# Kernel tuning notes

Measured on AMD Instinct MI355X. Metric: run time of the kernel, lower is better.

Reference implementation:

```python
import jax, jax.numpy as jnp
import numpy as np

B, T, D, HS = 8, 2048, 1024, 64


def setup_inputs() -> dict:
    key = jax.random.key(0)
    ks = jax.random.split(key, 7)
    return {
        "x": jax.random.normal(ks[0], (B, T, D), dtype=jnp.float32),
        "Wq": jax.random.normal(ks[1], (D, HS), dtype=jnp.float32) / np.sqrt(D),
        "bq": jax.random.normal(ks[2], (HS,), dtype=jnp.float32) * 0.01,
        "Wk": jax.random.normal(ks[3], (D, HS), dtype=jnp.float32) / np.sqrt(D),
        "bk": jax.random.normal(ks[4], (HS,), dtype=jnp.float32) * 0.01,
        "Wv": jax.random.normal(ks[5], (D, HS), dtype=jnp.float32) / np.sqrt(D),
        "bv": jax.random.normal(ks[6], (HS,), dtype=jnp.float32) * 0.01,
    }


def reference(x, Wq, bq, Wk, bk, Wv, bv):
    # Q,K,V projections: [B,T,D] @ [D,HS] -> [B,T,HS]
    Q = x @ Wq + bq
    K = x @ Wk + bk
    V = x @ Wv + bv
    # raw scores [B,T,T]
    scores = jnp.einsum("bqh,bkh->bqk", Q, K)
    # causal mask applied BEFORE scaling (as in the original; -inf is scale-invariant)
    causal = jnp.tril(jnp.ones((T, T), dtype=bool))
    scores = jnp.where(causal[None, :, :], scores, -jnp.inf)
    scores = scores / jnp.sqrt(jnp.asarray(HS, dtype=scores.dtype))
    attn = jax.nn.softmax(scores, axis=-1)
    # dropout is identity in eval mode (deterministic reference)
    return jnp.einsum("bqk,bkh->bqh", attn, V)
```

## Files before the change

kernel.cpp:

```cpp
#include <hip/hip_runtime.h>
#include <hip/hip_bf16.h>

typedef __bf16 bf16x8 __attribute__((ext_vector_type(8)));
typedef __bf16 bf16x4 __attribute__((ext_vector_type(4)));
typedef float  f32x4  __attribute__((ext_vector_type(4)));

#define B_  8
#define T_  2048
#define D_  1024
#define HS_ 64


__global__ __launch_bounds__(256) void pack_w(
    const float* __restrict__ Wq, const float* __restrict__ Wk,
    const float* __restrict__ Wv, __bf16* __restrict__ Wp)
{
    const int t    = blockIdx.x * 256 + threadIdx.x;
    const int lane = t & 63;
    const int pg   = t >> 6;
    const int s    = pg & 3;
    const int c    = (pg >> 2) & 31;
    const int p    = pg >> 7;
    const int m16  = lane & 15;
    const int quad = lane >> 4;

    const float* W = (p == 0) ? Wq : (p == 1) ? Wk : Wv;
    const float* src = W + (size_t)(c * 32 + quad * 8) * 64 + s * 16 + m16;
    bf16x8 frag;
    #pragma unroll
    for (int j = 0; j < 8; ++j) frag[j] = (__bf16)src[(size_t)j * 64];
    *(bf16x8*)(Wp + (size_t)pg * 512 + lane * 8) = frag;
}

__global__ __launch_bounds__(256) void qkv_fused(
    const float* __restrict__ x,
    const __bf16* __restrict__ Wp,
    const float* __restrict__ bq, const float* __restrict__ bk,
    const float* __restrict__ bv,
    __bf16* __restrict__ Q, __bf16* __restrict__ K, __bf16* __restrict__ Vt)
{
    __shared__ alignas(16) unsigned char Smem[36864];

    const int rt   = blockIdx.x;
    const int wave = threadIdx.x >> 6;
    const int lane = threadIdx.x & 63;
    const int m16  = lane & 15;
    const int quad = lane >> 4;
    const int row0 = rt * 16;

    __bf16* Xs = (__bf16*)(Smem + wave * 8448);

    {
        const float* xsrc = x + (size_t)row0 * 1024 + wave * 256;
        const int sr = lane >> 5;
        const int sc = (lane & 31) * 8;
        #pragma unroll
        for (int i = 0; i < 8; ++i) {
            const int r = i * 2 + sr;
            f32x4 v0 = *(const f32x4*)(xsrc + (size_t)r * 1024 + sc);
            f32x4 v1 = *(const f32x4*)(xsrc + (size_t)r * 1024 + sc + 4);
            bf16x8 w;
            #pragma unroll
            for (int e = 0; e < 4; ++e) { w[e] = (__bf16)v0[e]; w[4 + e] = (__bf16)v1[e]; }
            *(bf16x8*)&Xs[r * 264 + sc] = w;
        }
    }
    __builtin_amdgcn_wave_barrier();

    f32x4 acc[3][4];
    #pragma unroll
    for (int p = 0; p < 3; ++p)
        #pragma unroll
        for (int s = 0; s < 4; ++s) acc[p][s] = {0.f, 0.f, 0.f, 0.f};

    for (int k0 = 0; k0 < 256; k0 += 32) {
        bf16x8 a = *(const bf16x8*)&Xs[m16 * 264 + k0 + quad * 8];
        const int cbase = wave * 8 + (k0 >> 5);

        bf16x8 bf[12];
        #pragma unroll
        for (int ps = 0; ps < 12; ++ps) {
            const int p = ps >> 2, s = ps & 3;
            bf[ps] = *(const bf16x8*)(Wp +
                ((size_t)((p * 32 + cbase) * 4 + s) << 9) + lane * 8);
        }
        __builtin_amdgcn_sched_barrier(0);

        #pragma unroll
        for (int ps = 0; ps < 12; ++ps)
            acc[ps >> 2][ps & 3] =
                __builtin_amdgcn_mfma_f32_16x16x32_bf16(a, bf[ps], acc[ps >> 2][ps & 3], 0, 0, 0);
    }

    f32x4* Red = (f32x4*)Smem;
    __syncthreads();
    if (wave != 0) {
        #pragma unroll
        for (int p = 0; p < 3; ++p)
            #pragma unroll
            for (int s = 0; s < 4; ++s)
                Red[((wave - 1) * 12 + p * 4 + s) * 64 + lane] = acc[p][s];
    }
    __syncthreads();
    if (wave != 0) return;

    #pragma unroll
    for (int p = 0; p < 3; ++p)
        #pragma unroll
        for (int s = 0; s < 4; ++s) {
            f32x4 sum = acc[p][s];
            #pragma unroll
            for (int w = 0; w < 3; ++w) {
                f32x4 v = Red[(w * 12 + p * 4 + s) * 64 + lane];
                #pragma unroll
                for (int e = 0; e < 4; ++e) sum[e] += v[e];
            }
            acc[p][s] = sum;
        }

    #pragma unroll
    for (int s = 0; s < 4; ++s) {
        const int h = s * 16 + m16;
        const float bia = bq[h];
        #pragma unroll
        for (int r = 0; r < 4; ++r)
            Q[(size_t)(row0 + quad * 4 + r) * 64 + h] = (__bf16)(acc[0][s][r] + bia);
    }
    #pragma unroll
    for (int s = 0; s < 4; ++s) {
        const int h = s * 16 + m16;
        const float bia = bk[h];
        #pragma unroll
        for (int r = 0; r < 4; ++r)
            K[(size_t)(row0 + quad * 4 + r) * 64 + h] = (__bf16)(acc[1][s][r] + bia);
    }
    {
        const int bidx = row0 >> 11;
        const int t0   = (row0 & 2047) + quad * 4;
        #pragma unroll
        for (int s = 0; s < 4; ++s) {
            const int h = s * 16 + m16;
            const float bia = bv[h];
            bf16x4 pack;
            #pragma unroll
            for (int r = 0; r < 4; ++r) pack[r] = (__bf16)(acc[2][s][r] + bia);
            *(bf16x4*)(Vt + (size_t)bidx * (HS_ * T_) + (size_t)h * T_ + t0) = pack;
        }
    }
}

__global__ __launch_bounds__(256) void attn_fused(
    const __bf16* __restrict__ Q,
    const __bf16* __restrict__ K,
    const __bf16* __restrict__ Vt,
    float* __restrict__ O)
{
    __shared__ alignas(16) __bf16 Klds[8 * 512];
    __shared__ alignas(16) __bf16 Vlds[8 * 512];

    const int qt = blockIdx.x;
    const int b  = blockIdx.y;

    const int tid  = threadIdx.x;
    const int wave = tid >> 6;
    const int lane = tid & 63;
    const int m16  = lane & 15;
    const int quad = lane >> 4;

    const __bf16* Qb = Q  + (size_t)b * T_ * HS_;
    const __bf16* Kb = K  + (size_t)b * T_ * HS_;
    const __bf16* Vb = Vt + (size_t)b * HS_ * T_;

    const int q0   = qt * 64 + wave * 16;
    const int qrow = q0 + m16;

    bf16x8 qb0 = *(const bf16x8*)(Qb + (size_t)qrow * 64 + quad * 8);
    bf16x8 qb1 = *(const bf16x8*)(Qb + (size_t)qrow * 64 + 32 + quad * 8);

    int koffL[2], voffL[2];
    const __bf16* kgb[2];
    const __bf16* vgb[2];
    #pragma unroll
    for (int i = 0; i < 2; ++i) {
        const int p    = i * 256 + tid;
        const int trow = p >> 3;
        const int tcol = p & 7;
        const int snb  = ((trow >> 5) << 1) | ((trow >> 2) & 1);
        const int mk   = (((trow >> 3) & 3) << 2) | (trow & 3);
        koffL[i] = ((((snb << 1) | (tcol >> 2)) << 6) + (tcol & 3) * 16 + mk) * 8;
        voffL[i] = (((((trow >> 4) << 1) | (tcol >> 2)) << 6) + (tcol & 3) * 16 + (trow & 15)) * 8;
        kgb[i] = Kb + (size_t)trow * 64 + tcol * 8;
        vgb[i] = Vb + (size_t)trow * T_ + tcol * 8;
    }

    f32x4 o[4];
    #pragma unroll
    for (int hs = 0; hs < 4; ++hs) o[hs] = {0.f, 0.f, 0.f, 0.f};
    float m_run = -1e30f, l_run = 0.f;

    bf16x8 kr0 = *(const bf16x8*)(kgb[0]);
    bf16x8 kr1 = *(const bf16x8*)(kgb[1]);
    bf16x8 vr0 = *(const bf16x8*)(vgb[0]);
    bf16x8 vr1 = *(const bf16x8*)(vgb[1]);

    for (int jt = 0; jt <= qt; ++jt) {
        const int j0 = jt * 64;

        __syncthreads();
        *(bf16x8*)&Klds[koffL[0]] = kr0;
        *(bf16x8*)&Klds[koffL[1]] = kr1;
        *(bf16x8*)&Vlds[voffL[0]] = vr0;
        *(bf16x8*)&Vlds[voffL[1]] = vr1;
        __syncthreads();

        if (jt < qt) {
            const size_t nk = (size_t)(j0 + 64) * 64;
            kr0 = *(const bf16x8*)(kgb[0] + nk);
            kr1 = *(const bf16x8*)(kgb[1] + nk);
            vr0 = *(const bf16x8*)(vgb[0] + j0 + 64);
            vr1 = *(const bf16x8*)(vgb[1] + j0 + 64);
        }
        __builtin_amdgcn_sched_barrier(0);

        f32x4 s[4];
        #pragma unroll
        for (int snb = 0; snb < 4; ++snb) s[snb] = {0.f, 0.f, 0.f, 0.f};
        #pragma unroll
        for (int snb = 0; snb < 4; ++snb) {
            bf16x8 ka0 = *(const bf16x8*)&Klds[((snb * 2 + 0) * 64 + lane) * 8];
            bf16x8 ka1 = *(const bf16x8*)&Klds[((snb * 2 + 1) * 64 + lane) * 8];
            s[snb] = __builtin_amdgcn_mfma_f32_16x16x32_bf16(ka0, qb0, s[snb], 0, 0, 0);
            s[snb] = __builtin_amdgcn_mfma_f32_16x16x32_bf16(ka1, qb1, s[snb], 0, 0, 0);
        }

        float mx = -1e30f;
        #pragma unroll
        for (int snb = 0; snb < 4; ++snb) {
            const int kbase = j0 + ((snb >> 1) << 5) + (quad << 3) + ((snb & 1) << 2);
            #pragma unroll
            for (int r = 0; r < 4; ++r) {
                float v = s[snb][r] * 0.125f;
                v = (kbase + r <= qrow) ? v : -1e30f;
                s[snb][r] = v;
                mx = fmaxf(mx, v);
            }
        }
        mx = fmaxf(mx, __shfl_xor(mx, 16));
        mx = fmaxf(mx, __shfl_xor(mx, 32));

        const float newm  = fmaxf(m_run, mx);
        const float alpha = __expf(m_run - newm);
        m_run = newm;

        float rs = 0.f;
        #pragma unroll
        for (int snb = 0; snb < 4; ++snb)
            #pragma unroll
            for (int r = 0; r < 4; ++r) {
                float pv = __expf(s[snb][r] - newm);
                s[snb][r] = pv;
                rs += pv;
            }
        rs += __shfl_xor(rs, 16);
        rs += __shfl_xor(rs, 32);
        l_run = l_run * alpha + rs;

        #pragma unroll
        for (int hs = 0; hs < 4; ++hs)
            #pragma unroll
            for (int r = 0; r < 4; ++r) o[hs][r] *= alpha;

        bf16x8 pb0, pb1;
        #pragma unroll
        for (int r = 0; r < 4; ++r) {
            pb0[r]     = (__bf16)s[0][r];
            pb0[4 + r] = (__bf16)s[1][r];
            pb1[r]     = (__bf16)s[2][r];
            pb1[4 + r] = (__bf16)s[3][r];
        }

        #pragma unroll
        for (int hs = 0; hs < 4; ++hs) {
            bf16x8 va0 = *(const bf16x8*)&Vlds[((hs * 2 + 0) * 64 + lane) * 8];
            bf16x8 va1 = *(const bf16x8*)&Vlds[((hs * 2 + 1) * 64 + lane) * 8];
            o[hs] = __builtin_amdgcn_mfma_f32_16x16x32_bf16(va0, pb0, o[hs], 0, 0, 0);
            o[hs] = __builtin_amdgcn_mfma_f32_16x16x32_bf16(va1, pb1, o[hs], 0, 0, 0);
        }
    }

    const float inv = 1.f / l_run;
    float* Ob = O + ((size_t)b * T_ + (size_t)(qt * 64 + wave * 16 + m16)) * 64;
    #pragma unroll
    for (int hs = 0; hs < 4; ++hs) {
        f32x4 v;
        #pragma unroll
        for (int r = 0; r < 4; ++r) v[r] = o[hs][r] * inv;
        *(f32x4*)(Ob + hs * 16 + quad * 4) = v;
    }
}

extern "C" void kernel_launch(void* const* d_in, const int* in_sizes, int n_in,
                              void* d_out, int out_size, void* d_ws, size_t ws_size,
                              hipStream_t stream)
{
    const float* x  = (const float*)d_in[0];
    const float* Wq = (const float*)d_in[1];
    const float* bq = (const float*)d_in[2];
    const float* Wk = (const float*)d_in[3];
    const float* bk = (const float*)d_in[4];
    const float* Wv = (const float*)d_in[5];
    const float* bv = (const float*)d_in[6];
    float* out = (float*)d_out;

    __bf16* Wp = (__bf16*)d_ws;
    __bf16* Q  = Wp + 384 * 512;
    __bf16* K  = Q  + (size_t)B_ * T_ * HS_;
    __bf16* Vt = K  + (size_t)B_ * T_ * HS_;

    pack_w<<<96, 256, 0, stream>>>(Wq, Wk, Wv, Wp);
    qkv_fused<<<1024, 256, 0, stream>>>(x, Wp, bq, bk, bv, Q, K, Vt);
    attn_fused<<<dim3(32, 8), 256, 0, stream>>>(Q, K, Vt, out);
}
```

Baseline: 158.2 us.

## Balance causal attention work by pairing short and long query tiles per block

The attention kernel now uses 128-thread blocks that each handle 32 query rows. Each block processes two 32-row tiles in sequence, one early and one late (2*s and 126-2*s), so every block does about the same causal work instead of the last blocks doing far more. The LDS layout for K and V gains an XOR swizzle to cut bank conflicts on the MFMA operand reads. K/V tiles are shared by only 2 waves now, so reuse per load drops, and the grid still has only 256 blocks.

```diff
diff --git a/kernel.cpp b/kernel.cpp
--- a/kernel.cpp
+++ b/kernel.cpp
@@ -149,16 +149,16 @@
     }
 }
 
-__global__ __launch_bounds__(256) void attn_fused(
+__global__ __launch_bounds__(128) void attn_fused(
     const __bf16* __restrict__ Q,
     const __bf16* __restrict__ K,
     const __bf16* __restrict__ Vt,
     float* __restrict__ O)
 {
-    __shared__ alignas(16) __bf16 Klds[8 * 512];
-    __shared__ alignas(16) __bf16 Vlds[8 * 512];
-
-    const int qt = blockIdx.x;
+    __shared__ alignas(16) __bf16 Klds[4096];
+    __shared__ alignas(16) __bf16 Vlds[4096];
+
+    const int s  = blockIdx.x;
     const int b  = blockIdx.y;
 
     const int tid  = threadIdx.x;
@@ -170,133 +170,155 @@
     const __bf16* Qb = Q  + (size_t)b * T_ * HS_;
     const __bf16* Kb = K  + (size_t)b * T_ * HS_;
     const __bf16* Vb = Vt + (size_t)b * HS_ * T_;
-
-    const int q0   = qt * 64 + wave * 16;
-    const int qrow = q0 + m16;
-
-    bf16x8 qb0 = *(const bf16x8*)(Qb + (size_t)qrow * 64 + quad * 8);
-    bf16x8 qb1 = *(const bf16x8*)(Qb + (size_t)qrow * 64 + 32 + quad * 8);
-
-    int koffL[2], voffL[2];
-    const __bf16* kgb[2];
-    const __bf16* vgb[2];
-    #pragma unroll
-    for (int i = 0; i < 2; ++i) {
-        const int p    = i * 256 + tid;
-        const int trow = p >> 3;
-        const int tcol = p & 7;
+    float* Obase     = O  + (size_t)b * T_ * HS_;
+
+    const int tr0  = tid >> 3;
+    const int tcol = tid & 7;
+    const int c    = tcol & 3;
+    const int gco  = tcol >> 2;
+
+    int kOff[4], vOff[4];
+    #pragma unroll
+    for (int i = 0; i < 4; ++i) {
+        const int trow = tr0 + 16 * i;
         const int snb  = ((trow >> 5) << 1) | ((trow >> 2) & 1);
         const int mk   = (((trow >> 3) & 3) << 2) | (trow & 3);
-        koffL[i] = ((((snb << 1) | (tcol >> 2)) << 6) + (tcol & 3) * 16 + mk) * 8;
-        voffL[i] = (((((trow >> 4) << 1) | (tcol >> 2)) << 6) + (tcol & 3) * 16 + (trow & 15)) * 8;
+        const int ek   = (((snb << 1) | gco) << 9) + c * 128 + mk * 8;
+        kOff[i] = ek ^ (((ek >> 7) & 7) << 3);
+        const int ev   = ((((trow >> 4) << 1) | gco) << 9) + c * 128 + (trow & 15) * 8;
+        vOff[i] = ev ^ (((ev >> 7) & 7) << 3);
+    }
+    const __bf16* kgb[4];
+    const __bf16* vgb[4];
+    #pragma unroll
+    for (int i = 0; i < 4; ++i) {
+        const int trow = tr0 + 16 * i;
         kgb[i] = Kb + (size_t)trow * 64 + tcol * 8;
         vgb[i] = Vb + (size_t)trow * T_ + tcol * 8;
     }
 
-    f32x4 o[4];
-    #pragma unroll
-    for (int hs = 0; hs < 4; ++hs) o[hs] = {0.f, 0.f, 0.f, 0.f};
-    float m_run = -1e30f, l_run = 0.f;
-
-    bf16x8 kr0 = *(const bf16x8*)(kgb[0]);
-    bf16x8 kr1 = *(const bf16x8*)(kgb[1]);
-    bf16x8 vr0 = *(const bf16x8*)(vgb[0]);
-    bf16x8 vr1 = *(const bf16x8*)(vgb[1]);
-
-    for (int jt = 0; jt <= qt; ++jt) {
-        const int j0 = jt * 64;
-
-        __syncthreads();
-        *(bf16x8*)&Klds[koffL[0]] = kr0;
-        *(bf16x8*)&Klds[koffL[1]] = kr1;
-        *(bf16x8*)&Vlds[voffL[0]] = vr0;
-        *(bf16x8*)&Vlds[voffL[1]] = vr1;
-        __syncthreads();
-
-        if (jt < qt) {
-            const size_t nk = (size_t)(j0 + 64) * 64;
-            kr0 = *(const bf16x8*)(kgb[0] + nk);
-            kr1 = *(const bf16x8*)(kgb[1] + nk);
-            vr0 = *(const bf16x8*)(vgb[0] + j0 + 64);
-            vr1 = *(const bf16x8*)(vgb[1] + j0 + 64);
-        }
-        __builtin_amdgcn_sched_barrier(0);
-
-        f32x4 s[4];
-        #pragma unroll
-        for (int snb = 0; snb < 4; ++snb) s[snb] = {0.f, 0.f, 0.f, 0.f};
-        #pragma unroll
-        for (int snb = 0; snb < 4; ++snb) {
-            bf16x8 ka0 = *(const bf16x8*)&Klds[((snb * 2 + 0) * 64 + lane) * 8];
-            bf16x8 ka1 = *(const bf16x8*)&Klds[((snb * 2 + 1) * 64 + lane) * 8];
-            s[snb] = __builtin_amdgcn_mfma_f32_16x16x32_bf16(ka0, qb0, s[snb], 0, 0, 0);
-            s[snb] = __builtin_amdgcn_mfma_f32_16x16x32_bf16(ka1, qb1, s[snb], 0, 0, 0);
-        }
-
-        float mx = -1e30f;
-        #pragma unroll
-        for (int snb = 0; snb < 4; ++snb) {
-            const int kbase = j0 + ((snb >> 1) << 5) + (quad << 3) + ((snb & 1) << 2);
+    const int rsw0 = (lane * 8) ^ (quad << 3);
+    const int rsw1 = (lane * 8) ^ ((quad | 4) << 3);
+
+    auto phase = [&](const int h0) {
+        const int qrow  = (h0 + wave) * 16 + m16;
+        const int jtmax = h0 >> 2;
+
+        bf16x8 qb0 = *(const bf16x8*)(Qb + (size_t)qrow * 64 + quad * 8);
+        bf16x8 qb1 = *(const bf16x8*)(Qb + (size_t)qrow * 64 + 32 + quad * 8);
+
+        f32x4 o[4];
+        #pragma unroll
+        for (int hs = 0; hs < 4; ++hs) o[hs] = {0.f, 0.f, 0.f, 0.f};
+        float m_run = -1e30f, l_run = 0.f;
+
+        bf16x8 kr[4], vr[4];
+        #pragma unroll
+        for (int i = 0; i < 4; ++i) {
+            kr[i] = *(const bf16x8*)(kgb[i]);
+            vr[i] = *(const bf16x8*)(vgb[i]);
+        }
+
+        for (int jt = 0; jt <= jtmax; ++jt) {
+            const int j0 = jt * 64;
+
+            __syncthreads();
+            #pragma unroll
+            for (int i = 0; i < 4; ++i) {
+                *(bf16x8*)&Klds[kOff[i]] = kr[i];
+                *(bf16x8*)&Vlds[vOff[i]] = vr[i];
+            }
+            __syncthreads();
+
+            if (jt < jtmax) {
+                const size_t kadd = (size_t)(j0 + 64) * 64;
+                #pragma unroll
+                for (int i = 0; i < 4; ++i) {
+                    kr[i] = *(const bf16x8*)(kgb[i] + kadd);
+                    vr[i] = *(const bf16x8*)(vgb[i] + j0 + 64);
+                }
+            }
+            __builtin_amdgcn_sched_barrier(0);
+
+            f32x4 sv[4];
+            #pragma unroll
+            for (int snb = 0; snb < 4; ++snb) sv[snb] = {0.f, 0.f, 0.f, 0.f};
+            #pragma unroll
+            for (int snb = 0; snb < 4; ++snb) {
+                bf16x8 ka0 = *(const bf16x8*)&Klds[snb * 1024 + rsw0];
+                bf16x8 ka1 = *(const bf16x8*)&Klds[snb * 1024 + 512 + rsw1];
+                sv[snb] = __builtin_amdgcn_mfma_f32_16x16x32_bf16(ka0, qb0, sv[snb], 0, 0, 0);
+                sv[snb] = __builtin_amdgcn_mfma_f32_16x16x32_bf16(ka1, qb1, sv[snb], 0, 0, 0);
+            }
+
+            float mx = -1e30f;
+            #pragma unroll
+            for (int snb = 0; snb < 4; ++snb) {
+                const int kbase = j0 + ((snb >> 1) << 5) + (quad << 3) + ((snb & 1) << 2);
+                #pragma unroll
+                for (int r = 0; r < 4; ++r) {
+                    float v = sv[snb][r] * 0.125f;
+                    v = (kbase + r <= qrow) ? v : -1e30f;
+                    sv[snb][r] = v;
+                    mx = fmaxf(mx, v);
+                }
+            }
+            mx = fmaxf(mx, __shfl_xor(mx, 16));
+            mx = fmaxf(mx, __shfl_xor(mx, 32));
+
+            const float newm  = fmaxf(m_run, mx);
+            const float alpha = __expf(m_run - newm);
+            m_run = newm;
+
+            float rs = 0.f;
+            #pragma unroll
+            for (int snb = 0; snb < 4; ++snb)
+                #pragma unroll
+                for (int r = 0; r < 4; ++r) {
+                    float pv = __expf(sv[snb][r] - newm);
+                    sv[snb][r] = pv;
+                    rs += pv;
+                }
+            rs += __shfl_xor(rs, 16);
+            rs += __shfl_xor(rs, 32);
+            l_run = l_run * alpha + rs;
+
+            #pragma unroll
+            for (int hs = 0; hs < 4; ++hs)
+                #pragma unroll
+                for (int r = 0; r < 4; ++r) o[hs][r] *= alpha;
+
+            bf16x8 pb0, pb1;
             #pragma unroll
             for (int r = 0; r < 4; ++r) {
-                float v = s[snb][r] * 0.125f;
-                v = (kbase + r <= qrow) ? v : -1e30f;
-                s[snb][r] = v;
-                mx = fmaxf(mx, v);
-            }
-        }
-        mx = fmaxf(mx, __shfl_xor(mx, 16));
-        mx = fmaxf(mx, __shfl_xor(mx, 32));
-
-        const float newm  = fmaxf(m_run, mx);
-        const float alpha = __expf(m_run - newm);
-        m_run = newm;
-
-        float rs = 0.f;
-        #pragma unroll
-        for (int snb = 0; snb < 4; ++snb)
-            #pragma unroll
-            for (int r = 0; r < 4; ++r) {
-                float pv = __expf(s[snb][r] - newm);
-                s[snb][r] = pv;
-                rs += pv;
-            }
-        rs += __shfl_xor(rs, 16);
-        rs += __shfl_xor(rs, 32);
-        l_run = l_run * alpha + rs;
-
-        #pragma unroll
-        for (int hs = 0; hs < 4; ++hs)
-            #pragma unroll
-            for (int r = 0; r < 4; ++r) o[hs][r] *= alpha;
-
-        bf16x8 pb0, pb1;
-        #pragma unroll
-        for (int r = 0; r < 4; ++r) {
-            pb0[r]     = (__bf16)s[0][r];
-            pb0[4 + r] = (__bf16)s[1][r];
-            pb1[r]     = (__bf16)s[2][r];
-            pb1[4 + r] = (__bf16)s[3][r];
-        }
-
+                pb0[r]     = (__bf16)sv[0][r];
+                pb0[4 + r] = (__bf16)sv[1][r];
+                pb1[r]     = (__bf16)sv[2][r];
+                pb1[4 + r] = (__bf16)sv[3][r];
+            }
+
+            #pragma unroll
+            for (int hs = 0; hs < 4; ++hs) {
+                bf16x8 va0 = *(const bf16x8*)&Vlds[hs * 1024 + rsw0];
+                bf16x8 va1 = *(const bf16x8*)&Vlds[hs * 1024 + 512 + rsw1];
+                o[hs] = __builtin_amdgcn_mfma_f32_16x16x32_bf16(va0, pb0, o[hs], 0, 0, 0);
+                o[hs] = __builtin_amdgcn_mfma_f32_16x16x32_bf16(va1, pb1, o[hs], 0, 0, 0);
+            }
+        }
+
+        const float inv = 1.f / l_run;
+        float* Ob = Obase + (size_t)qrow * 64;
         #pragma unroll
         for (int hs = 0; hs < 4; ++hs) {
-            bf16x8 va0 = *(const bf16x8*)&Vlds[((hs * 2 + 0) * 64 + lane) * 8];
-            bf16x8 va1 = *(const bf16x8*)&Vlds[((hs * 2 + 1) * 64 + lane) * 8];
-            o[hs] = __builtin_amdgcn_mfma_f32_16x16x32_bf16(va0, pb0, o[hs], 0, 0, 0);
-            o[hs] = __builtin_amdgcn_mfma_f32_16x16x32_bf16(va1, pb1, o[hs], 0, 0, 0);
-        }
-    }
-
-    const float inv = 1.f / l_run;
-    float* Ob = O + ((size_t)b * T_ + (size_t)(qt * 64 + wave * 16 + m16)) * 64;
-    #pragma unroll
-    for (int hs = 0; hs < 4; ++hs) {
-        f32x4 v;
-        #pragma unroll
-        for (int r = 0; r < 4; ++r) v[r] = o[hs][r] * inv;
-        *(f32x4*)(Ob + hs * 16 + quad * 4) = v;
-    }
+            f32x4 v;
+            #pragma unroll
+            for (int r = 0; r < 4; ++r) v[r] = o[hs][r] * inv;
+            *(f32x4*)(Ob + hs * 16 + quad * 4) = v;
+        }
+    };
+
+    phase(2 * s);
+    phase(126 - 2 * s);
 }
 
 extern "C" void kernel_launch(void* const* d_in, const int* in_sizes, int n_in,
@@ -319,5 +341,5 @@
 
     pack_w<<<96, 256, 0, stream>>>(Wq, Wk, Wv, Wp);
     qkv_fused<<<1024, 256, 0, stream>>>(x, Wp, bq, bk, bv, Q, K, Vt);
-    attn_fused<<<dim3(32, 8), 256, 0, stream>>>(Q, K, Vt, out);
+    attn_fused<<<dim3(32, 8), 128, 0, stream>>>(Q, K, Vt, out);
 }
```

New measurement: 148.1 us. 1.07x faster.

## Pre-swizzle K/V into MFMA fragments and split attention KV tiles across waves

Applied to the files above, without the earlier changes.

The QKV kernel now writes K and V directly in MFMA-fragment order per 64-key tile, so the attention kernel can load operands straight from global memory into registers without LDS staging or barriers in the inner loop. Attention is restructured so each block handles two 16-row query groups (p and 127-p) for causal load balancing. Within each group, two waves split the key tiles (even and odd) and merge their partial softmax states through LDS. The causal mask is applied only on the diagonal tile, and exp2 with a folded scale replaces exp. Register pressure from double-buffered fragment arrays is higher, and each block now has only two waves, which lowers per-block parallelism.

```diff
diff --git a/kernel.cpp b/kernel.cpp
--- a/kernel.cpp
+++ b/kernel.cpp
@@ -37,7 +37,9 @@
     const __bf16* __restrict__ Wp,
     const float* __restrict__ bq, const float* __restrict__ bk,
     const float* __restrict__ bv,
-    __bf16* __restrict__ Q, __bf16* __restrict__ K, __bf16* __restrict__ Vt)
+    __bf16* __restrict__ Q,
+    __bf16* __restrict__ Kp,
+    __bf16* __restrict__ Vp)
 {
     __shared__ alignas(16) unsigned char Smem[36864];
 
@@ -126,177 +128,197 @@
         for (int r = 0; r < 4; ++r)
             Q[(size_t)(row0 + quad * 4 + r) * 64 + h] = (__bf16)(acc[0][s][r] + bia);
     }
-    #pragma unroll
-    for (int s = 0; s < 4; ++s) {
-        const int h = s * 16 + m16;
-        const float bia = bk[h];
-        #pragma unroll
-        for (int r = 0; r < 4; ++r)
-            K[(size_t)(row0 + quad * 4 + r) * 64 + h] = (__bf16)(acc[1][s][r] + bia);
-    }
+
+    const int tb = (row0 >> 4) & 3;
+    const int jt = (row0 >> 6) & 31;
+    const int bb = row0 >> 11;
+    __bf16* kpt = Kp + (((size_t)bb * 32 + jt) * 8) * 512;
+    __bf16* vpt = Vp + (((size_t)bb * 32 + jt) * 8) * 512;
+
     {
-        const int bidx = row0 >> 11;
-        const int t0   = (row0 & 2047) + quad * 4;
+        const int snb  = ((tb >> 1) << 1) | (quad & 1);
+        const int m16b = ((tb & 1) << 3) | ((quad >> 1) << 2);
+        #pragma unroll
+        for (int s = 0; s < 4; ++s) {
+            const int h = s * 16 + m16;
+            const float bia = bk[h];
+            const int g     = snb * 2 + (s >> 1);
+            const int quadc = ((s & 1) << 1) | (m16 >> 3);
+            const int j     = m16 & 7;
+            #pragma unroll
+            for (int r = 0; r < 4; ++r)
+                kpt[(size_t)g * 512 + (quadc * 16 + m16b + r) * 8 + j] =
+                    (__bf16)(acc[1][s][r] + bia);
+        }
+    }
+    {
+        const int lanec = ((((tb & 1) << 1) | (quad >> 1)) << 4) + m16;
+        const int jbase = (quad & 1) << 2;
         #pragma unroll
         for (int s = 0; s < 4; ++s) {
             const int h = s * 16 + m16;
             const float bia = bv[h];
+            const int g = s * 2 + (tb >> 1);
             bf16x4 pack;
             #pragma unroll
             for (int r = 0; r < 4; ++r) pack[r] = (__bf16)(acc[2][s][r] + bia);
-            *(bf16x4*)(Vt + (size_t)bidx * (HS_ * T_) + (size_t)h * T_ + t0) = pack;
+            *(bf16x4*)(vpt + (size_t)g * 512 + lanec * 8 + jbase) = pack;
         }
     }
 }
 
-__global__ __launch_bounds__(256) void attn_fused(
+__global__ __launch_bounds__(128) void attn_fused(
     const __bf16* __restrict__ Q,
-    const __bf16* __restrict__ K,
-    const __bf16* __restrict__ Vt,
+    const __bf16* __restrict__ Kp,
+    const __bf16* __restrict__ Vp,
     float* __restrict__ O)
 {
-    __shared__ alignas(16) __bf16 Klds[8 * 512];
-    __shared__ alignas(16) __bf16 Vlds[8 * 512];
-
-    const int qt = blockIdx.x;
+    __shared__ float Mrg[64][20];
+
+    const int p  = blockIdx.x;
     const int b  = blockIdx.y;
-
-    const int tid  = threadIdx.x;
-    const int wave = tid >> 6;
-    const int lane = tid & 63;
+    const int wave = threadIdx.x >> 6;
+    const int lane = threadIdx.x & 63;
     const int m16  = lane & 15;
     const int quad = lane >> 4;
+    const float SC = 0.18033688f;
 
     const __bf16* Qb = Q  + (size_t)b * T_ * HS_;
-    const __bf16* Kb = K  + (size_t)b * T_ * HS_;
-    const __bf16* Vb = Vt + (size_t)b * HS_ * T_;
-
-    const int q0   = qt * 64 + wave * 16;
-    const int qrow = q0 + m16;
-
-    bf16x8 qb0 = *(const bf16x8*)(Qb + (size_t)qrow * 64 + quad * 8);
-    bf16x8 qb1 = *(const bf16x8*)(Qb + (size_t)qrow * 64 + 32 + quad * 8);
-
-    int koffL[2], voffL[2];
-    const __bf16* kgb[2];
-    const __bf16* vgb[2];
-    #pragma unroll
-    for (int i = 0; i < 2; ++i) {
-        const int p    = i * 256 + tid;
-        const int trow = p >> 3;
-        const int tcol = p & 7;
-        const int snb  = ((trow >> 5) << 1) | ((trow >> 2) & 1);
-        const int mk   = (((trow >> 3) & 3) << 2) | (trow & 3);
-        koffL[i] = ((((snb << 1) | (tcol >> 2)) << 6) + (tcol & 3) * 16 + mk) * 8;
-        voffL[i] = (((((trow >> 4) << 1) | (tcol >> 2)) << 6) + (tcol & 3) * 16 + (trow & 15)) * 8;
-        kgb[i] = Kb + (size_t)trow * 64 + tcol * 8;
-        vgb[i] = Vb + (size_t)trow * T_ + tcol * 8;
-    }
-
-    f32x4 o[4];
-    #pragma unroll
-    for (int hs = 0; hs < 4; ++hs) o[hs] = {0.f, 0.f, 0.f, 0.f};
-    float m_run = -1e30f, l_run = 0.f;
-
-    bf16x8 kr0 = *(const bf16x8*)(kgb[0]);
-    bf16x8 kr1 = *(const bf16x8*)(kgb[1]);
-    bf16x8 vr0 = *(const bf16x8*)(vgb[0]);
-    bf16x8 vr1 = *(const bf16x8*)(vgb[1]);
-
-    for (int jt = 0; jt <= qt; ++jt) {
-        const int j0 = jt * 64;
-
+    const __bf16* Kb = Kp + (size_t)b * 32 * 4096;
+    const __bf16* Vb = Vp + (size_t)b * 32 * 4096;
+    float* Obase     = O  + (size_t)b * T_ * HS_;
+
+#define LOADT(KA, VA, JT)                                                  \
+    {                                                                      \
+        const __bf16* kb_ = Kb + (size_t)(JT) * 4096 + lane * 8;           \
+        const __bf16* vb_ = Vb + (size_t)(JT) * 4096 + lane * 8;           \
+        _Pragma("unroll")                                                  \
+        for (int g_ = 0; g_ < 8; ++g_) {                                   \
+            KA[g_] = *(const bf16x8*)(kb_ + g_ * 512);                     \
+            VA[g_] = *(const bf16x8*)(vb_ + g_ * 512);                     \
+        }                                                                  \
+    }
+
+#define STEP(CK, CV, NK, NV)                                               \
+    {                                                                      \
+        const int j0 = jt * 64;                                            \
+        f32x4 sv[4];                                                       \
+        _Pragma("unroll")                                                  \
+        for (int sn_ = 0; sn_ < 4; ++sn_) {                                \
+            sv[sn_] = {0.f, 0.f, 0.f, 0.f};                                \
+            sv[sn_] = __builtin_amdgcn_mfma_f32_16x16x32_bf16(CK[sn_*2],   qb0, sv[sn_], 0, 0, 0); \
+            sv[sn_] = __builtin_amdgcn_mfma_f32_16x16x32_bf16(CK[sn_*2+1], qb1, sv[sn_], 0, 0, 0); \
+        }                                                                  \
+        if (jt + 2 < ntiles) LOADT(NK, NV, jt + 2);                        \
+        __builtin_amdgcn_sched_barrier(0);                                 \
+        if (jt == ntiles - 1) {            \
+            _Pragma("unroll")                                              \
+            for (int sn_ = 0; sn_ < 4; ++sn_) {                            \
+                const int kbase = j0 + ((sn_ >> 1) << 5) + (quad << 3) + ((sn_ & 1) << 2); \
+                _Pragma("unroll")                                          \
+                for (int r_ = 0; r_ < 4; ++r_)                             \
+                    sv[sn_][r_] = (kbase + r_ <= qrow) ? sv[sn_][r_] : -3e38f; \
+            }                                                              \
+        }                                                                  \
+        float mx = -3e38f;                                                 \
+        _Pragma("unroll")                                                  \
+        for (int sn_ = 0; sn_ < 4; ++sn_)                                  \
+            _Pragma("unroll")                                              \
+            for (int r_ = 0; r_ < 4; ++r_) mx = fmaxf(mx, sv[sn_][r_]);    \
+        mx = fmaxf(mx, __shfl_xor(mx, 16));                                \
+        mx = fmaxf(mx, __shfl_xor(mx, 32));                                \
+        const float newm  = fmaxf(m_run, mx);                              \
+        const float alpha = exp2f((m_run - newm) * SC);                    \
+        m_run = newm;                                                      \
+        const float nm = newm * SC;                                        \
+        float rs = 0.f;                                                    \
+        _Pragma("unroll")                                                  \
+        for (int sn_ = 0; sn_ < 4; ++sn_)                                  \
+            _Pragma("unroll")                                              \
+            for (int r_ = 0; r_ < 4; ++r_) {                               \
+                float pv_ = exp2f(__builtin_fmaf(sv[sn_][r_], SC, -nm));   \
+                sv[sn_][r_] = pv_;                                         \
+                rs += pv_;                                                 \
+            }                                                              \
+        rs += __shfl_xor(rs, 16);                                          \
+        rs += __shfl_xor(rs, 32);                                          \
+        l_run = l_run * alpha + rs;                                        \
+        _Pragma("unroll")                                                  \
+        for (int hs_ = 0; hs_ < 4; ++hs_)                                  \
+            _Pragma("unroll")                                              \
+            for (int r_ = 0; r_ < 4; ++r_) o[hs_][r_] *= alpha;            \
+        bf16x8 pb0, pb1;                                                   \
+        _Pragma("unroll")                                                  \
+        for (int r_ = 0; r_ < 4; ++r_) {                                   \
+            pb0[r_]     = (__bf16)sv[0][r_];                               \
+            pb0[4 + r_] = (__bf16)sv[1][r_];                               \
+            pb1[r_]     = (__bf16)sv[2][r_];                               \
+            pb1[4 + r_] = (__bf16)sv[3][r_];                               \
+        }                                                                  \
+        _Pragma("unroll")                                                  \
+        for (int hs_ = 0; hs_ < 4; ++hs_) {                                \
+            o[hs_] = __builtin_amdgcn_mfma_f32_16x16x32_bf16(CV[hs_*2],   pb0, o[hs_], 0, 0, 0); \
+            o[hs_] = __builtin_amdgcn_mfma_f32_16x16x32_bf16(CV[hs_*2+1], pb1, o[hs_], 0, 0, 0); \
+        }                                                                  \
+    }
+
+    auto runPhase = [&](const int h) {
+        const int ntiles = (h >> 2) + 1;
+        const int qrow   = h * 16 + m16;
+
+        bf16x8 qb0 = *(const bf16x8*)(Qb + (size_t)qrow * 64 + quad * 8);
+        bf16x8 qb1 = *(const bf16x8*)(Qb + (size_t)qrow * 64 + 32 + quad * 8);
+
+        f32x4 o[4];
+        #pragma unroll
+        for (int hs = 0; hs < 4; ++hs) o[hs] = {0.f, 0.f, 0.f, 0.f};
+        float m_run = -3e38f, l_run = 0.f;
+
+        bf16x8 kA[8], vA[8], kB[8], vB[8];
+        int jt = wave;
+        if (jt < ntiles) {
+            LOADT(kA, vA, jt);
+            while (true) {
+                STEP(kA, vA, kB, vB);
+                jt += 2; if (jt >= ntiles) break;
+                STEP(kB, vB, kA, vA);
+                jt += 2; if (jt >= ntiles) break;
+            }
+        }
+
+        if (wave == 1) {
+            #pragma unroll
+            for (int hs = 0; hs < 4; ++hs)
+                #pragma unroll
+                for (int r = 0; r < 4; ++r) Mrg[lane][hs * 4 + r] = o[hs][r];
+            Mrg[lane][16] = m_run;
+            Mrg[lane][17] = l_run;
+        }
         __syncthreads();
-        *(bf16x8*)&Klds[koffL[0]] = kr0;
-        *(bf16x8*)&Klds[koffL[1]] = kr1;
-        *(bf16x8*)&Vlds[voffL[0]] = vr0;
-        *(bf16x8*)&Vlds[voffL[1]] = vr1;
+        if (wave == 0) {
+            const float m1 = Mrg[lane][16];
+            const float l1 = Mrg[lane][17];
+            const float M  = fmaxf(m_run, m1);
+            const float a0 = exp2f((m_run - M) * SC);
+            const float a1 = exp2f((m1 - M) * SC);
+            const float inv = 1.f / (l_run * a0 + l1 * a1);
+            float* Ob = Obase + (size_t)qrow * 64;
+            #pragma unroll
+            for (int hs = 0; hs < 4; ++hs) {
+                f32x4 v;
+                #pragma unroll
+                for (int r = 0; r < 4; ++r)
+                    v[r] = (o[hs][r] * a0 + Mrg[lane][hs * 4 + r] * a1) * inv;
+                *(f32x4*)(Ob + hs * 16 + quad * 4) = v;
+            }
+        }
         __syncthreads();
-
-        if (jt < qt) {
-            const size_t nk = (size_t)(j0 + 64) * 64;
-            kr0 = *(const bf16x8*)(kgb[0] + nk);
-            kr1 = *(const bf16x8*)(kgb[1] + nk);
-            vr0 = *(const bf16x8*)(vgb[0] + j0 + 64);
-            vr1 = *(const bf16x8*)(vgb[1] + j0 + 64);
-        }
-        __builtin_amdgcn_sched_barrier(0);
-
-        f32x4 s[4];
-        #pragma unroll
-        for (int snb = 0; snb < 4; ++snb) s[snb] = {0.f, 0.f, 0.f, 0.f};
-        #pragma unroll
-        for (int snb = 0; snb < 4; ++snb) {
-            bf16x8 ka0 = *(const bf16x8*)&Klds[((snb * 2 + 0) * 64 + lane) * 8];
-            bf16x8 ka1 = *(const bf16x8*)&Klds[((snb * 2 + 1) * 64 + lane) * 8];
-            s[snb] = __builtin_amdgcn_mfma_f32_16x16x32_bf16(ka0, qb0, s[snb], 0, 0, 0);
-            s[snb] = __builtin_amdgcn_mfma_f32_16x16x32_bf16(ka1, qb1, s[snb], 0, 0, 0);
-        }
-
-        float mx = -1e30f;
-        #pragma unroll
-        for (int snb = 0; snb < 4; ++snb) {
-            const int kbase = j0 + ((snb >> 1) << 5) + (quad << 3) + ((snb & 1) << 2);
-            #pragma unroll
-            for (int r = 0; r < 4; ++r) {
-                float v = s[snb][r] * 0.125f;
-                v = (kbase + r <= qrow) ? v : -1e30f;
-                s[snb][r] = v;
-                mx = fmaxf(mx, v);
-            }
-        }
-        mx = fmaxf(mx, __shfl_xor(mx, 16));
-        mx = fmaxf(mx, __shfl_xor(mx, 32));
-
-        const float newm  = fmaxf(m_run, mx);
-        const float alpha = __expf(m_run - newm);
-        m_run = newm;
-
-        float rs = 0.f;
-        #pragma unroll
-        for (int snb = 0; snb < 4; ++snb)
-            #pragma unroll
-            for (int r = 0; r < 4; ++r) {
-                float pv = __expf(s[snb][r] - newm);
-                s[snb][r] = pv;
-                rs += pv;
-            }
-        rs += __shfl_xor(rs, 16);
-        rs += __shfl_xor(rs, 32);
-        l_run = l_run * alpha + rs;
-
-        #pragma unroll
-        for (int hs = 0; hs < 4; ++hs)
-            #pragma unroll
-            for (int r = 0; r < 4; ++r) o[hs][r] *= alpha;
-
-        bf16x8 pb0, pb1;
-        #pragma unroll
-        for (int r = 0; r < 4; ++r) {
-            pb0[r]     = (__bf16)s[0][r];
-            pb0[4 + r] = (__bf16)s[1][r];
-            pb1[r]     = (__bf16)s[2][r];
-            pb1[4 + r] = (__bf16)s[3][r];
-        }
-
-        #pragma unroll
-        for (int hs = 0; hs < 4; ++hs) {
-            bf16x8 va0 = *(const bf16x8*)&Vlds[((hs * 2 + 0) * 64 + lane) * 8];
-            bf16x8 va1 = *(const bf16x8*)&Vlds[((hs * 2 + 1) * 64 + lane) * 8];
-            o[hs] = __builtin_amdgcn_mfma_f32_16x16x32_bf16(va0, pb0, o[hs], 0, 0, 0);
-            o[hs] = __builtin_amdgcn_mfma_f32_16x16x32_bf16(va1, pb1, o[hs], 0, 0, 0);
-        }
-    }
-
-    const float inv = 1.f / l_run;
-    float* Ob = O + ((size_t)b * T_ + (size_t)(qt * 64 + wave * 16 + m16)) * 64;
-    #pragma unroll
-    for (int hs = 0; hs < 4; ++hs) {
-        f32x4 v;
-        #pragma unroll
-        for (int r = 0; r < 4; ++r) v[r] = o[hs][r] * inv;
-        *(f32x4*)(Ob + hs * 16 + quad * 4) = v;
-    }
+    };
+
+    runPhase(p);
+    runPhase(127 - p);
+#undef STEP
+#undef LOADT
 }
 
 extern "C" void kernel_launch(void* const* d_in, const int* in_sizes, int n_in,
@@ -314,10 +336,10 @@
 
     __bf16* Wp = (__bf16*)d_ws;
     __bf16* Q  = Wp + 384 * 512;
-    __bf16* K  = Q  + (size_t)B_ * T_ * HS_;
-    __bf16* Vt = K  + (size_t)B_ * T_ * HS_;
+    __bf16* Kp = Q  + (size_t)B_ * T_ * HS_;
+    __bf16* Vp = Kp + (size_t)B_ * T_ * HS_;
 
     pack_w<<<96, 256, 0, stream>>>(Wq, Wk, Wv, Wp);
-    qkv_fused<<<1024, 256, 0, stream>>>(x, Wp, bq, bk, bv, Q, K, Vt);
-    attn_fused<<<dim3(32, 8), 256, 0, stream>>>(Q, K, Vt, out);
+    qkv_fused<<<1024, 256, 0, stream>>>(x, Wp, bq, bk, bv, Q, Kp, Vp);
+    attn_fused<<<dim3(64, 8), 128, 0, stream>>>(Q, Kp, Vp, out);
 }
```

After: 139.3 us. 12.0% less time.
